# Optimization experiments

Measured on AMD Instinct MI355X. Metric: run time of the kernel, lower is better.

Reference implementation:

```python
import jax, jax.numpy as jnp
import numpy as np

DIM = 2048
H = 16
HKV = 4
D = DIM // H          # 128 head_dim
ROPE_BASE = 10000.0
TRAIN_SEQ_LEN = 1024
EPS = float(np.finfo(np.float32).eps)  # torch F.rms_norm default eps


def setup_inputs() -> dict:
    key = jax.random.key(0)
    ks = jax.random.split(key, 6)
    B, T = 2, 2048
    return {
        "x": jax.random.normal(ks[0], (B, T, DIM), jnp.float32),
        "q_w": jax.random.normal(ks[1], (DIM, DIM), jnp.float32) * 0.02,
        "k_w": jax.random.normal(ks[2], (HKV * D, DIM), jnp.float32) * 0.02,
        "v_w": jax.random.normal(ks[3], (HKV * D, DIM), jnp.float32) * 0.02,
        "out_w": jax.random.normal(ks[4], (DIM, DIM), jnp.float32) * 0.02,
        "q_gain": jnp.ones((H,), jnp.float32),
    }


def _rope_tables(T, dtype):
    rd = D  # rope_dims == head_dim (rope_dims=0 in module)
    if T > TRAIN_SEQ_LEN:
        scale = T / TRAIN_SEQ_LEN
        base = ROPE_BASE * scale ** (rd / (rd - 2))
    else:
        base = ROPE_BASE
    inv_freq = 1.0 / base ** (np.arange(0, rd, 2, dtype=np.float32) / rd)
    t = np.arange(T, dtype=np.float32)
    freqs = np.outer(t, inv_freq)  # [T, rd/2]
    cos = jnp.asarray(np.cos(freqs), dtype)[None, :, None, :]  # [1,T,1,rd/2]
    sin = jnp.asarray(np.sin(freqs), dtype)[None, :, None, :]
    return cos, sin


def _rms_norm(x):
    var = jnp.mean(jnp.square(x), axis=-1, keepdims=True)
    return x * jax.lax.rsqrt(var + EPS)


def _apply_rotary(x, cos, sin):
    half = x.shape[-1] // 2
    x1, x2 = x[..., :half], x[..., half:]
    return jnp.concatenate((x1 * cos + x2 * sin, -x1 * sin + x2 * cos), axis=-1)


def reference(x, q_w, k_w, v_w, out_w, q_gain):
    B, T, dim = x.shape
    q = (x @ q_w.T).reshape(B, T, H, D)
    k = (x @ k_w.T).reshape(B, T, HKV, D)
    v = (x @ v_w.T).reshape(B, T, HKV, D)
    q = _rms_norm(q)
    k = _rms_norm(k)
    cos, sin = _rope_tables(T, q.dtype)
    q = _apply_rotary(q, cos, sin)
    k = _apply_rotary(k, cos, sin)
    q = q * q_gain[None, None, :, None]
    rep = H // HKV
    k_r = jnp.repeat(k, rep, axis=2)  # [B,T,H,D]
    v_r = jnp.repeat(v, rep, axis=2)
    scores = jnp.einsum('bqhd,bkhd->bhqk', q, k_r) / jnp.sqrt(jnp.asarray(D, q.dtype))
    causal = jnp.tril(jnp.ones((T, T), bool))
    scores = jnp.where(causal[None, None], scores, jnp.asarray(-jnp.inf, scores.dtype))
    p = jax.nn.softmax(scores, axis=-1)
    y = jnp.einsum('bhqk,bkhd->bqhd', p, v_r).reshape(B, T, dim)
    return y @ out_w.T
```

## Files before the change

### kernel.cpp

```cpp
#include <hip/hip_runtime.h>
#include <hip/hip_bf16.h>

typedef __bf16 bf16x8 __attribute__((ext_vector_type(8)));
typedef unsigned short u16x8 __attribute__((ext_vector_type(8)));
typedef float f32x4 __attribute__((ext_vector_type(4)));
typedef __hip_bfloat16 bf16;

#define GLOAD_LDS16(g, l)                                               \
  __builtin_amdgcn_global_load_lds(                                     \
      (__attribute__((address_space(1))) void*)(void*)(g),              \
      (__attribute__((address_space(3))) void*)(void*)(l), 16, 0, 0)

__global__ __launch_bounds__(256) void cvt_all(
    const float4* __restrict__ x,  const float4* __restrict__ qw,
    const float4* __restrict__ kw, const float4* __restrict__ vw,
    const float4* __restrict__ ow,
    ushort4* __restrict__ xb,  ushort4* __restrict__ qwb,
    ushort4* __restrict__ kwb, ushort4* __restrict__ vwb,
    ushort4* __restrict__ owb)
{
  const int i = blockIdx.x * 256 + threadIdx.x;
  const float4* s; ushort4* d; int off;
  if      (i < 2097152) { s = x;  d = xb;  off = i; }
  else if (i < 3145728) { s = qw; d = qwb; off = i - 2097152; }
  else if (i < 3407872) { s = kw; d = kwb; off = i - 3145728; }
  else if (i < 3670016) { s = vw; d = vwb; off = i - 3407872; }
  else                  { s = ow; d = owb; off = i - 3670016; }
  float4 v = s[off];
  bf16 b0 = __float2bfloat16(v.x), b1 = __float2bfloat16(v.y);
  bf16 b2 = __float2bfloat16(v.z), b3 = __float2bfloat16(v.w);
  ushort4 o;
  o.x = *(unsigned short*)&b0; o.y = *(unsigned short*)&b1;
  o.z = *(unsigned short*)&b2; o.w = *(unsigned short*)&b3;
  d[off] = o;
}

__device__ __forceinline__ void store_out(bf16* p, float v)  { *p = __float2bfloat16(v); }
__device__ __forceinline__ void store_out(float* p, float v) { *p = v; }

template <typename OutT>
__device__ __forceinline__ void gemm_tile_body(
    const bf16* __restrict__ A, const bf16* __restrict__ W, OutT* __restrict__ C,
    int bm, int bn, int N, int K, bf16* As, bf16* Ws)
{
  const int tid  = threadIdx.x;
  const int lane = tid & 63;
  const int wave = tid >> 6;
  const int wm = (wave >> 1) * 64;
  const int wn = (wave & 1) * 64;
  const int mfrag = lane & 15;
  const int kfrag = (lane >> 4) * 8;

  f32x4 acc[4][4] = {};

  for (int k0 = 0; k0 < K; k0 += 32) {
#pragma unroll
    for (int r = 0; r < 2; ++r) {
      const int off  = r * 4096 + wave * 1024 + lane * 16;
      const int row  = off >> 6;
      const int colb = off & 63;
      const char* ga = (const char*)A + ((size_t)(bm + row) * K + k0) * 2 + colb;
      GLOAD_LDS16(ga, (char*)As + r * 4096 + wave * 1024);
      const char* gw = (const char*)W + ((size_t)(bn + row) * K + k0) * 2 + colb;
      GLOAD_LDS16(gw, (char*)Ws + r * 4096 + wave * 1024);
    }
    __syncthreads();

    bf16x8 af[4], wf[4];
#pragma unroll
    for (int i = 0; i < 4; ++i)
      af[i] = *(const bf16x8*)(As + (wm + i * 16 + mfrag) * 32 + kfrag);
#pragma unroll
    for (int j = 0; j < 4; ++j)
      wf[j] = *(const bf16x8*)(Ws + (wn + j * 16 + mfrag) * 32 + kfrag);
#pragma unroll
    for (int i = 0; i < 4; ++i)
#pragma unroll
      for (int j = 0; j < 4; ++j)
        acc[i][j] = __builtin_amdgcn_mfma_f32_16x16x32_bf16(af[i], wf[j], acc[i][j], 0, 0, 0);
    __syncthreads();
  }

  const int rq = (lane >> 4) * 4;
#pragma unroll
  for (int i = 0; i < 4; ++i)
#pragma unroll
    for (int j = 0; j < 4; ++j)
#pragma unroll
      for (int r = 0; r < 4; ++r) {
        const int row = bm + wm + i * 16 + rq + r;
        const int col = bn + wn + j * 16 + mfrag;
        store_out(&C[(size_t)row * N + col], acc[i][j][r]);
      }
}

__global__ __launch_bounds__(256) void gemm_bt_f32out(
    const bf16* __restrict__ A, const bf16* __restrict__ W, float* __restrict__ C,
    int N, int K)
{
  __shared__ bf16 As[128 * 32];
  __shared__ bf16 Ws[128 * 32];
  gemm_tile_body<float>(A, W, C, blockIdx.y * 128, blockIdx.x * 128, N, K, As, Ws);
}

__global__ __launch_bounds__(256) void gemm_qkv(
    const bf16* __restrict__ X, const bf16* __restrict__ Wq,
    const bf16* __restrict__ Wk, const bf16* __restrict__ Wv,
    bf16* __restrict__ Qo, bf16* __restrict__ Ko, bf16* __restrict__ Vo, int K)
{
  __shared__ bf16 As[128 * 32];
  __shared__ bf16 Ws[128 * 32];
  const int bx = blockIdx.x;
  const bf16* W; bf16* C; int N, bn;
  if (bx < 16)      { W = Wq; C = Qo; N = 2048; bn = bx * 128; }
  else if (bx < 20) { W = Wk; C = Ko; N = 512;  bn = (bx - 16) * 128; }
  else              { W = Wv; C = Vo; N = 512;  bn = (bx - 20) * 128; }
  gemm_tile_body<bf16>(X, W, C, blockIdx.y * 128, bn, N, K, As, Ws);
}

__device__ __forceinline__ void rope_row(
    bf16* __restrict__ buf, const float* __restrict__ gain,
    int nh, float scale, int row)
{
  const int j = threadIdx.x & 63;
  const int bt = row / nh;
  const int h  = row - bt * nh;
  const int t  = bt & 2047;
  bf16* p = buf + (size_t)bt * (nh * 128) + h * 128;

  float x1 = __bfloat162float(p[j]);
  float x2 = __bfloat162float(p[j + 64]);
  float ss = x1 * x1 + x2 * x2;
#pragma unroll
  for (int off = 32; off > 0; off >>= 1) ss += __shfl_xor(ss, off, 64);
  const float rinv = rsqrtf(ss * (1.0f / 128.0f) + 1.1920928955078125e-07f);
  const float g = gain ? gain[h] : 1.0f;
  const float s = rinv * g * scale;

  const float inv_freq = exp2f(-(float)j * (14.3035853954f / 64.0f));
  const float fr = (float)t * inv_freq;
  const float cs = cosf(fr), sn = sinf(fr);
  p[j]      = __float2bfloat16(s * (x1 * cs + x2 * sn));
  p[j + 64] = __float2bfloat16(s * (x2 * cs - x1 * sn));
}

__global__ __launch_bounds__(256) void postqkv(
    bf16* __restrict__ qb, bf16* __restrict__ kb,
    const unsigned short* __restrict__ vb, unsigned short* __restrict__ vtb,
    const float* __restrict__ gain)
{
  const int bx = blockIdx.x;
  if (bx < 16384) {
    rope_row(qb, gain, 16, 0.08838834764831845f, bx * 4 + (threadIdx.x >> 6));
  } else if (bx < 20480) {
    rope_row(kb, nullptr, 4, 1.0f, (bx - 16384) * 4 + (threadIdx.x >> 6));
  } else {
    const int idx = (bx - 20480) * 256 + threadIdx.x;
    const int t  = idx & 4095;
    const int dc = idx >> 12;
    u16x8 v = *(const u16x8*)(vb + (size_t)t * 512 + dc * 8);
#pragma unroll
    for (int j = 0; j < 8; ++j)
      vtb[(size_t)(dc * 8 + j) * 4096 + t] = v[j];
  }
}

__global__ __launch_bounds__(256) void flash_attn(
    const bf16* __restrict__ Q, const bf16* __restrict__ Kg,
    const bf16* __restrict__ Vtg, bf16* __restrict__ Y)
{
  __shared__ bf16 Ks[2][64 * 128];
  __shared__ bf16 Vs[2][128 * 64];
  __shared__ bf16 Ps[4][16 * 64];

  const int tid = threadIdx.x, lane = tid & 63, w = tid >> 6;
  const int p = blockIdx.x & 15, bh = blockIdx.x >> 4;
  const int h = bh & 15, b = bh >> 4, kvh = h >> 2;
  const int mfrag = lane & 15, quad = lane >> 4;
  const int m7 = mfrag & 7;

  auto stage_k = [&](int kt, int s) {
#pragma unroll
    for (int g = 0; g < 4; ++g) {
      const int o = g * 4096 + w * 1024 + lane * 16;
      const int r = o >> 8, c = (o >> 4) & 15;
      const int cs = (c & 8) | ((c ^ (r & 7)) & 7);
      const bf16* src = Kg + ((size_t)(b * 2048 + kt * 64 + r)) * 512 + kvh * 128 + cs * 8;
      GLOAD_LDS16(src, (char*)&Ks[s][0] + g * 4096 + w * 1024);
    }
  };
  auto stage_v = [&](int kt, int s) {
#pragma unroll
    for (int g = 0; g < 4; ++g) {
      const int o = g * 4096 + w * 1024 + lane * 16;
      const int r = o >> 7, c = (o >> 4) & 7;
      const int cs = (c ^ (r & 7)) & 7;
      const bf16* src = Vtg + ((size_t)(kvh * 128 + r)) * 4096 + b * 2048 + kt * 64 + cs * 8;
      GLOAD_LDS16(src, (char*)&Vs[s][0] + g * 4096 + w * 1024);
    }
  };

  stage_k(0, 0);
  stage_v(0, 0);
  int sb = 0;
  bf16* psw = &Ps[w][0];

  for (int phase = 0; phase < 2; ++phase) {
    const int qt = phase ? p : 31 - p;

    bf16x8 qf[4];
    const bf16* qrow = Q + ((size_t)(b * 2048 + qt * 64 + w * 16 + mfrag)) * 2048 + h * 128;
#pragma unroll
    for (int c = 0; c < 4; ++c) qf[c] = *(const bf16x8*)(qrow + c * 32 + quad * 8);

    f32x4 oacc[8] = {};
    float l_lane[4] = {0.f, 0.f, 0.f, 0.f};
    const int q_base = qt * 64 + w * 16 + quad * 4;

    for (int kt = 0; kt <= qt; ++kt) {
      __syncthreads();
      const bool last = (phase == 1) && (kt == qt);
      if (!last) {
        const int nk = kt < qt ? kt + 1 : 0;
        stage_k(nk, sb ^ 1);
        stage_v(nk, sb ^ 1);
      }

      f32x4 sc[4] = {};
#pragma unroll
      for (int kc = 0; kc < 4; ++kc) {
        const bf16* krow = &Ks[sb][0] + (kc * 16 + mfrag) * 128;
#pragma unroll
        for (int c = 0; c < 4; ++c) {
          const int G = 4 * c + quad;
          const int cs = (G & 8) | ((G ^ m7) & 7);
          bf16x8 kf = *(const bf16x8*)(krow + cs * 8);
          sc[kc] = __builtin_amdgcn_mfma_f32_16x16x32_bf16(qf[c], kf, sc[kc], 0, 0, 0);
        }
      }

      if (kt == qt) {
        const int kcol0 = kt * 64 + mfrag;
#pragma unroll
        for (int kc = 0; kc < 4; ++kc)
#pragma unroll
          for (int r = 0; r < 4; ++r)
            if (kcol0 + kc * 16 > q_base + r) sc[kc][r] = -1e30f;
      }

#pragma unroll
      for (int kc = 0; kc < 4; ++kc)
#pragma unroll
        for (int r = 0; r < 4; ++r) {
          const float pv = __expf(sc[kc][r] - 14.0f);
          l_lane[r] += pv;
          const int q = quad * 4 + r;
          const int slot = ((2 * kc + (mfrag >> 3)) ^ (q & 7)) & 7;
          psw[q * 64 + slot * 8 + m7] = __float2bfloat16(pv);
        }

#pragma unroll
      for (int kh = 0; kh < 2; ++kh) {
        const int Gp = 4 * kh + quad;
        const int sl = (Gp ^ m7) & 7;
        bf16x8 pf = *(const bf16x8*)(psw + mfrag * 64 + sl * 8);
#pragma unroll
        for (int dc = 0; dc < 8; ++dc) {
          bf16x8 vf = *(const bf16x8*)(&Vs[sb][0] + (dc * 16 + mfrag) * 64 + sl * 8);
          oacc[dc] = __builtin_amdgcn_mfma_f32_16x16x32_bf16(pf, vf, oacc[dc], 0, 0, 0);
        }
      }
      sb ^= 1;
    }

#pragma unroll
    for (int r = 0; r < 4; ++r) {
      float l = l_lane[r];
      l += __shfl_xor(l, 1, 64);
      l += __shfl_xor(l, 2, 64);
      l += __shfl_xor(l, 4, 64);
      l += __shfl_xor(l, 8, 64);
      const float linv = 1.0f / l;
      const size_t row = (size_t)(b * 2048 + q_base + r);
#pragma unroll
      for (int dc = 0; dc < 8; ++dc)
        Y[row * 2048 + h * 128 + dc * 16 + mfrag] = __float2bfloat16(oacc[dc][r] * linv);
    }
  }
}

extern "C" void kernel_launch(void* const* d_in, const int* in_sizes, int n_in,
                              void* d_out, int out_size, void* d_ws, size_t ws_size,
                              hipStream_t stream)
{
  const float* x      = (const float*)d_in[0];
  const float* q_w    = (const float*)d_in[1];
  const float* k_w    = (const float*)d_in[2];
  const float* v_w    = (const float*)d_in[3];
  const float* o_w    = (const float*)d_in[4];
  const float* q_gain = (const float*)d_in[5];
  float* out = (float*)d_out;

  char* ws = (char*)d_ws;
  bf16* xb  = (bf16*)(ws);
  bf16* yb  = (bf16*)(ws);
  bf16* qwb = (bf16*)(ws + (16u << 20));
  bf16* vtb = (bf16*)(ws + (16u << 20));
  bf16* owb = (bf16*)(ws + (24u << 20));
  bf16* kwb = (bf16*)(ws + (32u << 20));
  bf16* vwb = (bf16*)(ws + (34u << 20));
  bf16* qb  = (bf16*)(ws + (36u << 20));
  bf16* kb  = (bf16*)(ws + (52u << 20));
  bf16* vb  = (bf16*)(ws + (56u << 20));

  const dim3 blk(256);
  cvt_all<<<dim3(18432), blk, 0, stream>>>(
      (const float4*)x, (const float4*)q_w, (const float4*)k_w,
      (const float4*)v_w, (const float4*)o_w,
      (ushort4*)xb, (ushort4*)qwb, (ushort4*)kwb, (ushort4*)vwb, (ushort4*)owb);

  gemm_qkv<<<dim3(24, 32), blk, 0, stream>>>(xb, qwb, kwb, vwb, qb, kb, vb, 2048);

  postqkv<<<dim3(21504), blk, 0, stream>>>(
      qb, kb, (const unsigned short*)vb, (unsigned short*)vtb, q_gain);

  flash_attn<<<dim3(512), blk, 0, stream>>>(qb, kb, vtb, yb);

  gemm_bt_f32out<<<dim3(16, 32), blk, 0, stream>>>(yb, owb, out, 2048, 2048);
}
```

Before: 323.8 us.

## Share K/V tiles across two GQA heads per block using 32x32 MFMA

```diff
diff --git a/kernel.cpp b/kernel.cpp
--- a/kernel.cpp
+++ b/kernel.cpp
@@ -4,6 +4,7 @@
 typedef __bf16 bf16x8 __attribute__((ext_vector_type(8)));
 typedef unsigned short u16x8 __attribute__((ext_vector_type(8)));
 typedef float f32x4 __attribute__((ext_vector_type(4)));
+typedef float f32x16 __attribute__((ext_vector_type(16)));
 typedef __hip_bfloat16 bf16;
 
 #define GLOAD_LDS16(g, l)                                               \
@@ -165,19 +166,23 @@
   }
 }
 
-__global__ __launch_bounds__(256) void flash_attn(
+__global__ __launch_bounds__(256, 1) void flash_attn(
     const bf16* __restrict__ Q, const bf16* __restrict__ Kg,
     const bf16* __restrict__ Vtg, bf16* __restrict__ Y)
 {
   __shared__ bf16 Ks[2][64 * 128];
   __shared__ bf16 Vs[2][128 * 64];
-  __shared__ bf16 Ps[4][16 * 64];
-
-  const int tid = threadIdx.x, lane = tid & 63, w = tid >> 6;
-  const int p = blockIdx.x & 15, bh = blockIdx.x >> 4;
-  const int h = bh & 15, b = bh >> 4, kvh = h >> 2;
-  const int mfrag = lane & 15, quad = lane >> 4;
-  const int m7 = mfrag & 7;
+  __shared__ bf16 Ps[4][32 * 64];
+
+  const int tid  = threadIdx.x, lane = tid & 63, w = tid >> 6;
+  const int p    = blockIdx.x & 15;
+  const int hp   = (blockIdx.x >> 4) & 1;
+  const int kvh  = (blockIdx.x >> 5) & 3;
+  const int b    = blockIdx.x >> 7;
+  const int hA   = kvh * 4 + hp * 2;
+  const int l31  = lane & 31;
+  const int half = lane >> 5;
+  const int l7   = lane & 7;
 
   auto stage_k = [&](int kt, int s) {
 #pragma unroll
@@ -208,14 +213,19 @@
   for (int phase = 0; phase < 2; ++phase) {
     const int qt = phase ? p : 31 - p;
 
-    bf16x8 qf[4];
-    const bf16* qrow = Q + ((size_t)(b * 2048 + qt * 64 + w * 16 + mfrag)) * 2048 + h * 128;
-#pragma unroll
-    for (int c = 0; c < 4; ++c) qf[c] = *(const bf16x8*)(qrow + c * 32 + quad * 8);
-
-    f32x4 oacc[8] = {};
-    float l_lane[4] = {0.f, 0.f, 0.f, 0.f};
-    const int q_base = qt * 64 + w * 16 + quad * 4;
+    bf16x8 qf[8];
+    {
+      const bf16* qrow = Q + ((size_t)(b * 2048 + qt * 64 + w * 16 + (l31 & 15))) * 2048
+                           + (hA + (l31 >> 4)) * 128 + half * 8;
+#pragma unroll
+      for (int c = 0; c < 8; ++c) qf[c] = *(const bf16x8*)(qrow + c * 16);
+    }
+
+    f32x16 oacc[4] = {};
+    float l_lane[16];
+#pragma unroll
+    for (int r = 0; r < 16; ++r) l_lane[r] = 0.f;
+    const int qb0 = qt * 64 + w * 16;
 
     for (int kt = 0; kt <= qt; ++kt) {
       __syncthreads();
@@ -226,65 +236,71 @@
         stage_v(nk, sb ^ 1);
       }
 
-      f32x4 sc[4] = {};
-#pragma unroll
-      for (int kc = 0; kc < 4; ++kc) {
-        const bf16* krow = &Ks[sb][0] + (kc * 16 + mfrag) * 128;
-#pragma unroll
-        for (int c = 0; c < 4; ++c) {
-          const int G = 4 * c + quad;
-          const int cs = (G & 8) | ((G ^ m7) & 7);
+      f32x16 sc[2] = {};
+#pragma unroll
+      for (int kb = 0; kb < 2; ++kb) {
+        const bf16* krow = &Ks[sb][0] + (kb * 32 + l31) * 128;
+#pragma unroll
+        for (int c = 0; c < 8; ++c) {
+          const int G = c * 2 + half;
+          const int cs = (G & 8) | ((G ^ l7) & 7);
           bf16x8 kf = *(const bf16x8*)(krow + cs * 8);
-          sc[kc] = __builtin_amdgcn_mfma_f32_16x16x32_bf16(qf[c], kf, sc[kc], 0, 0, 0);
+          sc[kb] = __builtin_amdgcn_mfma_f32_32x32x16_bf16(qf[c], kf, sc[kb], 0, 0, 0);
         }
       }
 
       if (kt == qt) {
-        const int kcol0 = kt * 64 + mfrag;
-#pragma unroll
-        for (int kc = 0; kc < 4; ++kc)
-#pragma unroll
-          for (int r = 0; r < 4; ++r)
-            if (kcol0 + kc * 16 > q_base + r) sc[kc][r] = -1e30f;
-      }
-
-#pragma unroll
-      for (int kc = 0; kc < 4; ++kc)
-#pragma unroll
-        for (int r = 0; r < 4; ++r) {
-          const float pv = __expf(sc[kc][r] - 14.0f);
+#pragma unroll
+        for (int kb = 0; kb < 2; ++kb) {
+          const int key = kt * 64 + kb * 32 + l31;
+#pragma unroll
+          for (int r = 0; r < 16; ++r) {
+            const int row = (r & 3) + 8 * (r >> 2) + 4 * half;
+            if (key > qb0 + (row & 15)) sc[kb][r] = -1e30f;
+          }
+        }
+      }
+
+#pragma unroll
+      for (int kb = 0; kb < 2; ++kb)
+#pragma unroll
+        for (int r = 0; r < 16; ++r) {
+          const float pv = __expf(sc[kb][r] - 14.0f);
           l_lane[r] += pv;
-          const int q = quad * 4 + r;
-          const int slot = ((2 * kc + (mfrag >> 3)) ^ (q & 7)) & 7;
-          psw[q * 64 + slot * 8 + m7] = __float2bfloat16(pv);
+          const int row  = (r & 3) + 8 * (r >> 2) + 4 * half;
+          const int key  = kb * 32 + l31;
+          const int slot = ((key >> 3) ^ (row & 7)) & 7;
+          psw[row * 64 + slot * 8 + (key & 7)] = __float2bfloat16(pv);
         }
 
 #pragma unroll
-      for (int kh = 0; kh < 2; ++kh) {
-        const int Gp = 4 * kh + quad;
-        const int sl = (Gp ^ m7) & 7;
-        bf16x8 pf = *(const bf16x8*)(psw + mfrag * 64 + sl * 8);
-#pragma unroll
-        for (int dc = 0; dc < 8; ++dc) {
-          bf16x8 vf = *(const bf16x8*)(&Vs[sb][0] + (dc * 16 + mfrag) * 64 + sl * 8);
-          oacc[dc] = __builtin_amdgcn_mfma_f32_16x16x32_bf16(pf, vf, oacc[dc], 0, 0, 0);
+      for (int c2 = 0; c2 < 4; ++c2) {
+        const int sl = ((c2 * 2 + half) ^ l7) & 7;
+        bf16x8 pf = *(const bf16x8*)(psw + l31 * 64 + sl * 8);
+#pragma unroll
+        for (int db = 0; db < 4; ++db) {
+          bf16x8 vf = *(const bf16x8*)(&Vs[sb][0] + (db * 32 + l31) * 64 + sl * 8);
+          oacc[db] = __builtin_amdgcn_mfma_f32_32x32x16_bf16(pf, vf, oacc[db], 0, 0, 0);
         }
       }
       sb ^= 1;
     }
 
 #pragma unroll
-    for (int r = 0; r < 4; ++r) {
+    for (int r = 0; r < 16; ++r) {
       float l = l_lane[r];
       l += __shfl_xor(l, 1, 64);
       l += __shfl_xor(l, 2, 64);
       l += __shfl_xor(l, 4, 64);
       l += __shfl_xor(l, 8, 64);
+      l += __shfl_xor(l, 16, 64);
       const float linv = 1.0f / l;
-      const size_t row = (size_t)(b * 2048 + q_base + r);
-#pragma unroll
-      for (int dc = 0; dc < 8; ++dc)
-        Y[row * 2048 + h * 128 + dc * 16 + mfrag] = __float2bfloat16(oacc[dc][r] * linv);
+      const int row = (r & 3) + 8 * (r >> 2) + 4 * half;
+      bf16* yp = Y + ((size_t)(b * 2048 + qb0 + (row & 15))) * 2048
+                   + (hA + (row >> 4)) * 128 + l31;
+#pragma unroll
+      for (int db = 0; db < 4; ++db)
+        yp[db * 32] = __float2bfloat16(oacc[db][r] * linv);
     }
   }
 }
@@ -324,7 +340,7 @@
   postqkv<<<dim3(21504), blk, 0, stream>>>(
       qb, kb, (const unsigned short*)vb, (unsigned short*)vtb, q_gain);
 
-  flash_attn<<<dim3(512), blk, 0, stream>>>(qb, kb, vtb, yb);
+  flash_attn<<<dim3(256), blk, 0, stream>>>(qb, kb, vtb, yb);
 
   gemm_bt_f32out<<<dim3(16, 32), blk, 0, stream>>>(yb, owb, out, 2048, 2048);
 }
```

After: 332.1 us. 1.03x slower.
